# Optimization experiments

Hardware: AMD Instinct MI355X
Metric: run time of the kernel (lower is better)

## Reference

```python
import jax, jax.numpy as jnp
import numpy as np

B, N, C = 2, 2048, 1024
H = 16
D = C // H  # 64
EPS = 1e-6


def rms_norm(x, w):
    # LlamaRMSNorm: fp32 variance over last dim
    xf = x.astype(jnp.float32)
    var = jnp.mean(xf * xf, axis=-1, keepdims=True)
    xf = xf * jax.lax.rsqrt(var + EPS)
    return (w * xf).astype(x.dtype)


def setup_inputs() -> dict:
    key = jax.random.key(0)
    ks = jax.random.split(key, 4)
    x = jax.random.normal(ks[0], (B, N, C), dtype=jnp.float32)
    mask = jax.random.randint(ks[1], (B, N), 0, 2, dtype=jnp.int32)
    qkv_w = jax.random.normal(ks[2], (3 * C, C), dtype=jnp.float32) * (1.0 / np.sqrt(C))
    qkv_b = jnp.zeros((3 * C,), dtype=jnp.float32)
    proj_w = jax.random.normal(ks[3], (C, C), dtype=jnp.float32) * (1.0 / np.sqrt(C))
    proj_b = jnp.zeros((C,), dtype=jnp.float32)
    qn_w = jnp.ones((D,), dtype=jnp.float32)
    kn_w = jnp.ones((D,), dtype=jnp.float32)
    return {"x": x, "mask": mask, "qkv_w": qkv_w, "qkv_b": qkv_b,
            "proj_w": proj_w, "proj_b": proj_b, "qn_w": qn_w, "kn_w": kn_w}


def reference(x, mask, qkv_w, qkv_b, proj_w, proj_b, qn_w, kn_w):
    dtype = x.dtype
    scale = D ** -0.5
    # qkv projection -> (3, B, H, N, D)
    qkv = (x @ qkv_w.T + qkv_b).reshape(B, N, 3, H, D).transpose(2, 0, 3, 1, 4)
    q, k, v = qkv[0], qkv[1], qkv[2]
    q = rms_norm(q, qn_w)
    k = rms_norm(k, kn_w)
    q = q * scale
    # scores in fp32, key-padding mask [B,1,1,N]
    attn = jnp.einsum('bhnd,bhmd->bhnm', q, k).astype(jnp.float32)
    key_mask = (mask != 0)[:, None, None, :]
    attn = jnp.where(key_mask, attn, jnp.float32(-1e9))
    attn = jax.nn.softmax(attn, axis=-1).astype(dtype)
    out = jnp.einsum('bhnm,bhmd->bhnd', attn, v)  # (B,H,N,D)
    out = out.transpose(0, 2, 1, 3).reshape(B, N, C)
    return out @ proj_w.T + proj_b
```

## Files before the change

kernel.cpp:

```cpp
#include <hip/hip_runtime.h>
#include <hip/hip_bf16.h>
#include <stdint.h>
#include <math.h>

namespace {

constexpr int kB = 2;
constexpr int kN = 2048;
constexpr int kC = 1024;
constexpr int kH = 16;
constexpr int kD = 64;
constexpr int kTok = kB * kN;
constexpr int k3C  = 3 * kC;
constexpr size_t kPS = (size_t)kTok * k3C;
constexpr size_t kXE = (size_t)kTok * kC;
constexpr size_t kWQ = (size_t)k3C * kC;
constexpr size_t kWP = (size_t)kC * kC;

using bhalf8 = __attribute__((ext_vector_type(8))) __bf16;
using f32x4  = __attribute__((ext_vector_type(4))) float;

__device__ inline unsigned short f2bf(float f) {
  __hip_bfloat16 h = __float2bfloat16(f);
  return *reinterpret_cast<unsigned short*>(&h);
}
__device__ inline float bf2f(unsigned short u) {
  __hip_bfloat16 h;
  *reinterpret_cast<unsigned short*>(&h) = u;
  return __bfloat162float(h);
}
__device__ inline void split2(float v, unsigned short& h, unsigned short& l) {
  const unsigned short hb = f2bf(v);
  h = hb;
  l = f2bf(v - bf2f(hb));
}

#if __has_builtin(__builtin_amdgcn_exp2f)
__device__ inline float fexp2(float x) { return __builtin_amdgcn_exp2f(x); }
#else
__device__ inline float fexp2(float x) { return __expf(x * 0.6931471805599453f); }
#endif

__device__ inline void glds16(const unsigned short* g, unsigned short* l) {
  __builtin_amdgcn_global_load_lds(
      (const __attribute__((address_space(1))) void*)g,
      (__attribute__((address_space(3))) void*)l, 16, 0, 0);
}

__device__ inline void split4(const float4 v, ushort4& hh, ushort4& ll) {
  split2(v.x, hh.x, ll.x); split2(v.y, hh.y, ll.y);
  split2(v.z, hh.z, ll.z); split2(v.w, hh.w, ll.w);
}

__global__ __launch_bounds__(256)
void prep_split(const float* __restrict__ x, const float* __restrict__ wq,
                unsigned short* __restrict__ xH, unsigned short* __restrict__ xL,
                unsigned short* __restrict__ wqH, unsigned short* __restrict__ wqL)
{
  constexpr int nX = (int)(kXE / 4);
  int i = blockIdx.x * 256 + threadIdx.x;
  const float* src;
  unsigned short *H, *L;
  if (i < nX) { src = x;  H = xH;  L = xL; }
  else        { i -= nX; src = wq; H = wqH; L = wqL; }
  const float4 v = ((const float4*)src)[i];
  ushort4 hh, ll;
  split4(v, hh, ll);
  ((ushort4*)H)[i] = hh;
  ((ushort4*)L)[i] = ll;
}

__global__ __launch_bounds__(256)
void vt_and_split(const unsigned short* __restrict__ H,
                  unsigned short* __restrict__ VTH,
                  const float* __restrict__ wp,
                  unsigned short* __restrict__ wpH,
                  unsigned short* __restrict__ wpL)
{
  if (blockIdx.x < 2048) {
    const int gw   = blockIdx.x * 4 + (threadIdx.x >> 6);
    const int lane = threadIdx.x & 63;
    const int bh   = gw >> 8;
    const int oct  = gw & 255;
    const int b = bh >> 4, h = bh & 15;
    const int tok0 = oct * 8;
    union { unsigned short u[8]; uint4 v; } ph;
    #pragma unroll
    for (int e = 0; e < 8; ++e) {
      const size_t g = (size_t)(b * kN + tok0 + e) * k3C + 2 * kC + h * kD + lane;
      ph.u[e] = H[g];
    }
    *(uint4*)(&VTH[((size_t)bh * kD + lane) * kN + tok0]) = ph.v;
  } else {
    const int i = (blockIdx.x - 2048) * 256 + threadIdx.x;
    const float4 v = ((const float4*)wp)[i];
    ushort4 hh, ll;
    split4(v, hh, ll);
    ((ushort4*)wpH)[i] = hh;
    ((ushort4*)wpL)[i] = ll;
  }
}

__global__ __launch_bounds__(512)
void gemm_qkv256(const unsigned short* __restrict__ AH,
                 const unsigned short* __restrict__ AL,
                 const unsigned short* __restrict__ WH,
                 const unsigned short* __restrict__ WL,
                 const float* __restrict__ bias,
                 unsigned short* __restrict__ OutH,
                 unsigned short* __restrict__ OutL,
                 const float* __restrict__ qn,
                 const float* __restrict__ kn)
{
  constexpr int BK = 32;
  constexpr int NT = kC / BK;

  __shared__ __align__(16) unsigned short sA[2][2][256 * 32];
  __shared__ __align__(16) unsigned short sB[2][2][256 * 32];

  const int tt   = threadIdx.x;
  const int wave = tt >> 6;
  const int lane = tt & 63;
  const int quad = lane >> 4;
  const int l16  = lane & 15;
  const int bm = blockIdx.x * 256;
  const int bn = blockIdx.y * 256;
  const int wm = (wave >> 2) * 128;
  const int wn = (wave & 3) * 64;

  int srow[2], scol[2];
  #pragma unroll
  for (int r = 0; r < 2; ++r) {
    const int u = r * 512 + tt;
    srow[r] = u >> 2;
    scol[r] = ((u & 3) ^ ((srow[r] >> 1) & 3)) * 8;
  }

  auto stageU = [&](int bf, int k0, int which) {
    const unsigned short* src = (which == 0) ? AH : (which == 1) ? WH
                              : (which == 2) ? WL : AL;
    const int base = (which == 0 || which == 3) ? bm : bn;
    unsigned short* dst = (which == 0) ? &sA[bf][0][0]
                        : (which == 3) ? &sA[bf][1][0]
                        : (which == 1) ? &sB[bf][0][0] : &sB[bf][1][0];
    #pragma unroll
    for (int r = 0; r < 2; ++r)
      glds16(&src[(size_t)(base + srow[r]) * kC + k0 + scol[r]],
             &dst[(r * 512 + tt) * 8]);
  };

  auto rdA = [&](int bf, int pl, int row) -> bhalf8 {
    return *(const bhalf8*)(&sA[bf][pl][row * 32 + ((quad ^ ((row >> 1) & 3)) * 8)]);
  };
  auto rdB = [&](int bf, int pl, int row) -> bhalf8 {
    return *(const bhalf8*)(&sB[bf][pl][row * 32 + ((quad ^ ((row >> 1) & 3)) * 8)]);
  };

  f32x4 acc[8][4] = {};
  bhalf8 ah[8], bh_[4], bl_[4];

  stageU(0, 0, 0); stageU(0, 0, 1); stageU(0, 0, 2); stageU(0, 0, 3);
  asm volatile("s_waitcnt vmcnt(4)" ::: "memory");
  __builtin_amdgcn_sched_barrier(0);
  asm volatile("s_barrier" ::: "memory");

  for (int t = 0; t < NT - 1; ++t) {
    const int buf  = t & 1;
    const int nbuf = buf ^ 1;
    const int nk0  = (t + 1) * BK;

    #pragma unroll
    for (int i = 0; i < 8; ++i) ah[i]  = rdA(buf, 0, wm + i * 16 + l16);
    #pragma unroll
    for (int j = 0; j < 4; ++j) bh_[j] = rdB(buf, 0, wn + j * 16 + l16);
    stageU(nbuf, nk0, 0);
    stageU(nbuf, nk0, 1);
    asm volatile("s_waitcnt vmcnt(6)" ::: "memory");
    __builtin_amdgcn_sched_barrier(0);
    asm volatile("s_barrier" ::: "memory");
    __builtin_amdgcn_s_setprio(1);
    #pragma unroll
    for (int i = 0; i < 8; ++i)
      #pragma unroll
      for (int j = 0; j < 4; ++j)
        acc[i][j] = __builtin_amdgcn_mfma_f32_16x16x32_bf16(ah[i], bh_[j], acc[i][j], 0, 0, 0);
    __builtin_amdgcn_s_setprio(0);

    #pragma unroll
    for (int j = 0; j < 4; ++j) bl_[j] = rdB(buf, 1, wn + j * 16 + l16);
    stageU(nbuf, nk0, 2);
    asm volatile("s_waitcnt vmcnt(6)" ::: "memory");
    __builtin_amdgcn_sched_barrier(0);
    asm volatile("s_barrier" ::: "memory");
    __builtin_amdgcn_s_setprio(1);
    #pragma unroll
    for (int i = 0; i < 8; ++i)
      #pragma unroll
      for (int j = 0; j < 4; ++j)
        acc[i][j] = __builtin_amdgcn_mfma_f32_16x16x32_bf16(ah[i], bl_[j], acc[i][j], 0, 0, 0);
    __builtin_amdgcn_s_setprio(0);

    stageU(nbuf, nk0, 3);
    asm volatile("s_waitcnt vmcnt(4)" ::: "memory");
    __builtin_amdgcn_sched_barrier(0);
    asm volatile("s_barrier" ::: "memory");
    __builtin_amdgcn_s_setprio(1);
    {
      bhalf8 al0[4];
      #pragma unroll
      for (int i = 0; i < 4; ++i) al0[i] = rdA(buf, 1, wm + i * 16 + l16);
      #pragma unroll
      for (int i = 0; i < 4; ++i)
        #pragma unroll
        for (int j = 0; j < 4; ++j)
          acc[i][j] = __builtin_amdgcn_mfma_f32_16x16x32_bf16(al0[i], bh_[j], acc[i][j], 0, 0, 0);
      bhalf8 al1[4];
      #pragma unroll
      for (int i = 0; i < 4; ++i) al1[i] = rdA(buf, 1, wm + (4 + i) * 16 + l16);
      #pragma unroll
      for (int i = 0; i < 4; ++i)
        #pragma unroll
        for (int j = 0; j < 4; ++j)
          acc[4 + i][j] = __builtin_amdgcn_mfma_f32_16x16x32_bf16(al1[i], bh_[j], acc[4 + i][j], 0, 0, 0);
    }
    __builtin_amdgcn_s_setprio(0);
    asm volatile("s_barrier" ::: "memory");
  }

  {
    const int buf = (NT - 1) & 1;
    #pragma unroll
    for (int i = 0; i < 8; ++i) ah[i]  = rdA(buf, 0, wm + i * 16 + l16);
    #pragma unroll
    for (int j = 0; j < 4; ++j) bh_[j] = rdB(buf, 0, wn + j * 16 + l16);
    __builtin_amdgcn_s_setprio(1);
    #pragma unroll
    for (int i = 0; i < 8; ++i)
      #pragma unroll
      for (int j = 0; j < 4; ++j)
        acc[i][j] = __builtin_amdgcn_mfma_f32_16x16x32_bf16(ah[i], bh_[j], acc[i][j], 0, 0, 0);
    __builtin_amdgcn_s_setprio(0);

    asm volatile("s_waitcnt vmcnt(2)" ::: "memory");
    __builtin_amdgcn_sched_barrier(0);
    asm volatile("s_barrier" ::: "memory");
    #pragma unroll
    for (int j = 0; j < 4; ++j) bl_[j] = rdB(buf, 1, wn + j * 16 + l16);
    __builtin_amdgcn_s_setprio(1);
    #pragma unroll
    for (int i = 0; i < 8; ++i)
      #pragma unroll
      for (int j = 0; j < 4; ++j)
        acc[i][j] = __builtin_amdgcn_mfma_f32_16x16x32_bf16(ah[i], bl_[j], acc[i][j], 0, 0, 0);
    __builtin_amdgcn_s_setprio(0);

    asm volatile("s_waitcnt vmcnt(0)" ::: "memory");
    __builtin_amdgcn_sched_barrier(0);
    asm volatile("s_barrier" ::: "memory");
    __builtin_amdgcn_s_setprio(1);
    {
      bhalf8 al0[4];
      #pragma unroll
      for (int i = 0; i < 4; ++i) al0[i] = rdA(buf, 1, wm + i * 16 + l16);
      #pragma unroll
      for (int i = 0; i < 4; ++i)
        #pragma unroll
        for (int j = 0; j < 4; ++j)
          acc[i][j] = __builtin_amdgcn_mfma_f32_16x16x32_bf16(al0[i], bh_[j], acc[i][j], 0, 0, 0);
      bhalf8 al1[4];
      #pragma unroll
      for (int i = 0; i < 4; ++i) al1[i] = rdA(buf, 1, wm + (4 + i) * 16 + l16);
      #pragma unroll
      for (int i = 0; i < 4; ++i)
        #pragma unroll
        for (int j = 0; j < 4; ++j)
          acc[4 + i][j] = __builtin_amdgcn_mfma_f32_16x16x32_bf16(al1[i], bh_[j], acc[4 + i][j], 0, 0, 0);
    }
    __builtin_amdgcn_s_setprio(0);
  }

  const int slice = bn >> 10;
  const bool writeL = (slice == 0);
  float bv[4], wv[4];
  #pragma unroll
  for (int j = 0; j < 4; ++j) {
    bv[j] = bias[bn + wn + j * 16 + l16];
    if (slice < 2) wv[j] = (slice ? kn : qn)[j * 16 + l16];
  }

  #pragma unroll
  for (int i = 0; i < 8; ++i) {
    float val[4][4];
    #pragma unroll
    for (int j = 0; j < 4; ++j)
      #pragma unroll
      for (int r = 0; r < 4; ++r)
        val[j][r] = acc[i][j][r] + bv[j];

    if (slice < 2) {
      #pragma unroll
      for (int r = 0; r < 4; ++r) {
        float ss = val[0][r] * val[0][r];
        #pragma unroll
        for (int j = 1; j < 4; ++j) ss += val[j][r] * val[j][r];
        #pragma unroll
        for (int d = 1; d < 16; d <<= 1) ss += __shfl_xor(ss, d, 64);
        float rinv = rsqrtf(ss * (1.0f / 64.0f) + 1e-6f);
        if (slice == 0) rinv *= 0.18033688011112042f;
        #pragma unroll
        for (int j = 0; j < 4; ++j) val[j][r] = wv[j] * (val[j][r] * rinv);
      }
    }

    #pragma unroll
    for (int j = 0; j < 4; ++j) {
      const int n = bn + wn + j * 16 + l16;
      #pragma unroll
      for (int r = 0; r < 4; ++r) {
        const int m = bm + wm + i * 16 + quad * 4 + r;
        unsigned short hh, ll;
        split2(val[j][r], hh, ll);
        OutH[(size_t)m * k3C + n] = hh;
        if (writeL) OutL[(size_t)m * k3C + n] = ll;
      }
    }
  }
}

template<bool OUTF32, bool FUSE_NORM>
__global__ __launch_bounds__(256)
void gemm_planes(const unsigned short* __restrict__ AH,
                 const unsigned short* __restrict__ AL, int lda,
                 const unsigned short* __restrict__ WH,
                 const unsigned short* __restrict__ WL,
                 const float* __restrict__ bias,
                 float* __restrict__ OutF,
                 unsigned short* __restrict__ OutH,
                 unsigned short* __restrict__ OutL,
                 const float* __restrict__ qn,
                 const float* __restrict__ kn,
                 int Nn, int K)
{
  __shared__ __align__(16) unsigned short AsH[128 * 32], AsL[128 * 32];
  __shared__ __align__(16) unsigned short BsH[128 * 32], BsL[128 * 32];

  const int t    = threadIdx.x;
  const int wave = t >> 6;
  const int lane = t & 63;
  const int quad = lane >> 4;
  const int l16  = lane & 15;
  const int bm = blockIdx.x * 128;
  const int bn = blockIdx.y * 128;
  const int wm = (wave >> 1) * 64;
  const int wn = (wave & 1) * 64;

  f32x4 acc[4][4] = {};

  for (int k0 = 0; k0 < K; k0 += 32) {
    #pragma unroll
    for (int r = 0; r < 2; ++r) {
      const int c   = r * 256 + t;
      const int row = c >> 2;
      const int col = (c & 3) * 8;
      glds16(&AH[(size_t)(bm + row) * lda + k0 + col], &AsH[c * 8]);
      glds16(&AL[(size_t)(bm + row) * lda + k0 + col], &AsL[c * 8]);
      glds16(&WH[(size_t)(bn + row) * K + k0 + col], &BsH[c * 8]);
      glds16(&WL[(size_t)(bn + row) * K + k0 + col], &BsL[c * 8]);
    }
    __syncthreads();

    bhalf8 afh[4], afl[4], bgh[4], bgl[4];
    #pragma unroll
    for (int i = 0; i < 4; ++i) {
      afh[i] = *(const bhalf8*)(&AsH[(wm + i * 16 + l16) * 32 + quad * 8]);
      afl[i] = *(const bhalf8*)(&AsL[(wm + i * 16 + l16) * 32 + quad * 8]);
      bgh[i] = *(const bhalf8*)(&BsH[(wn + i * 16 + l16) * 32 + quad * 8]);
      bgl[i] = *(const bhalf8*)(&BsL[(wn + i * 16 + l16) * 32 + quad * 8]);
    }
    #pragma unroll
    for (int i = 0; i < 4; ++i)
      #pragma unroll
      for (int j = 0; j < 4; ++j) {
        f32x4 a = acc[i][j];
        a = __builtin_amdgcn_mfma_f32_16x16x32_bf16(afh[i], bgh[j], a, 0, 0, 0);
        a = __builtin_amdgcn_mfma_f32_16x16x32_bf16(afh[i], bgl[j], a, 0, 0, 0);
        a = __builtin_amdgcn_mfma_f32_16x16x32_bf16(afl[i], bgh[j], a, 0, 0, 0);
        acc[i][j] = a;
      }
    __syncthreads();
  }

  float bv[4], wv[4];
  const int slice = FUSE_NORM ? (bn >> 10) : 0;
  const bool writeL = !FUSE_NORM || slice == 0;
  #pragma unroll
  for (int j = 0; j < 4; ++j) {
    bv[j] = bias[bn + wn + j * 16 + l16];
    if (FUSE_NORM && slice < 2)
      wv[j] = (slice ? kn : qn)[j * 16 + l16];
  }

  #pragma unroll
  for (int i = 0; i < 4; ++i) {
    float val[4][4];
    #pragma unroll
    for (int j = 0; j < 4; ++j)
      #pragma unroll
      for (int r = 0; r < 4; ++r)
        val[j][r] = acc[i][j][r] + bv[j];

    if (FUSE_NORM && slice < 2) {
      #pragma unroll
      for (int r = 0; r < 4; ++r) {
        float ss = val[0][r] * val[0][r];
        #pragma unroll
        for (int j = 1; j < 4; ++j) ss += val[j][r] * val[j][r];
        #pragma unroll
        for (int d = 1; d < 16; d <<= 1) ss += __shfl_xor(ss, d, 64);
        float rinv = rsqrtf(ss * (1.0f / 64.0f) + 1e-6f);
        if (slice == 0) rinv *= 0.125f;
        #pragma unroll
        for (int j = 0; j < 4; ++j) val[j][r] = wv[j] * (val[j][r] * rinv);
      }
    }

    #pragma unroll
    for (int j = 0; j < 4; ++j) {
      const int n = bn + wn + j * 16 + l16;
      #pragma unroll
      for (int r = 0; r < 4; ++r) {
        const int m = bm + wm + i * 16 + quad * 4 + r;
        if (OUTF32) {
          OutF[(size_t)m * Nn + n] = val[j][r];
        } else {
          unsigned short hh, ll;
          split2(val[j][r], hh, ll);
          OutH[(size_t)m * Nn + n] = hh;
          if (writeL) OutL[(size_t)m * Nn + n] = ll;
        }
      }
    }
  }
}

__global__ __launch_bounds__(256)
void attn_kernel(unsigned short* __restrict__ H, unsigned short* __restrict__ L,
                 const unsigned short* __restrict__ VTH,
                 const int* __restrict__ mask)
{
  constexpr int P   = 72;
  constexpr int Ppt = 68;
  __shared__ __align__(16) unsigned short KtH[2][64 * P];
  __shared__ __align__(16) unsigned short VtH[2][64 * P];
  __shared__ __align__(16) unsigned short Pt[4][32 * Ppt];

  const int t    = threadIdx.x;
  const int wave = t >> 6;
  const int lane = t & 63;
  const int quad = lane >> 4;
  const int l16  = lane & 15;

  const int lin  = blockIdx.x;
  const int xcd  = lin & 7;
  const int slot = lin >> 3;
  const int bh   = xcd + 8 * (slot >> 4);
  const int qblk = slot & 15;
  const int b  = bh >> 4;
  const int h  = bh & 15;
  const int q0 = qblk * 128 + wave * 32;

  const int row0 = t >> 3,         col0 = (t & 7) * 8;
  const int row1 = (256 + t) >> 3, col1 = ((256 + t) & 7) * 8;

  bhalf8 qfh[2][2], qfl[2][2];
  #pragma unroll
  for (int g = 0; g < 2; ++g) {
    const size_t qrow = (size_t)(b * kN + q0 + g * 16 + l16) * k3C + h * kD;
    qfh[g][0] = *(const bhalf8*)(&H[qrow + quad * 8]);
    qfh[g][1] = *(const bhalf8*)(&H[qrow + 32 + quad * 8]);
    qfl[g][0] = *(const bhalf8*)(&L[qrow + quad * 8]);
    qfl[g][1] = *(const bhalf8*)(&L[qrow + 32 + quad * 8]);
  }

  f32x4 acc_o[2][4] = {};
  float lpart[2][4] = {};

  uint4 sk0, sk1, sv0, sv1;
  int mcur[4], mnext[4];

  auto pref = [&](int kt) {
    sk0 = *(const uint4*)(&H[(size_t)(b * kN + kt + row0) * k3C + kC + h * kD + col0]);
    sk1 = *(const uint4*)(&H[(size_t)(b * kN + kt + row1) * k3C + kC + h * kD + col1]);
    sv0 = *(const uint4*)(&VTH[((size_t)bh * kD + row0) * kN + kt + col0]);
    sv1 = *(const uint4*)(&VTH[((size_t)bh * kD + row1) * kN + kt + col1]);
  };
  auto store_tile = [&](int bf) {
    *(uint4*)(&KtH[bf][row0 * P + col0]) = sk0;
    *(uint4*)(&KtH[bf][row1 * P + col1]) = sk1;
    *(uint4*)(&VtH[bf][row0 * P + col0]) = sv0;
    *(uint4*)(&VtH[bf][row1 * P + col1]) = sv1;
  };
  auto loadM = [&](int kt, int* m) {
    #pragma unroll
    for (int nt = 0; nt < 4; ++nt) m[nt] = mask[b * kN + kt + nt * 16 + l16];
  };

  pref(0);
  loadM(0, mcur);
  #pragma unroll
  for (int nt = 0; nt < 4; ++nt) mnext[nt] = mcur[nt];
  store_tile(0);
  pref(64);
  __syncthreads();

  for (int i = 0; i < 32; ++i) {
    const int cur = i & 1;
    const int kt = i * 64;
    if (i < 31) loadM(kt + 64, mnext);

    #pragma unroll
    for (int nt = 0; nt < 4; ++nt) {
      const int kr = (nt * 16 + l16) * P + quad * 8;
      const bhalf8 kh0 = *(const bhalf8*)(&KtH[cur][kr]);
      const bhalf8 kh1 = *(const bhalf8*)(&KtH[cur][kr + 32]);
      const float flag = mcur[nt] ? 1.0f : 0.0f;
      #pragma unroll
      for (int g = 0; g < 2; ++g) {
        f32x4 s = {};
        s = __builtin_amdgcn_mfma_f32_16x16x32_bf16(qfh[g][0], kh0, s, 0, 0, 0);
        s = __builtin_amdgcn_mfma_f32_16x16x32_bf16(qfh[g][1], kh1, s, 0, 0, 0);
        s = __builtin_amdgcn_mfma_f32_16x16x32_bf16(qfl[g][0], kh0, s, 0, 0, 0);
        s = __builtin_amdgcn_mfma_f32_16x16x32_bf16(qfl[g][1], kh1, s, 0, 0, 0);
        #pragma unroll
        for (int r = 0; r < 4; ++r) {
          const float p = flag * fexp2(s[r]);
          lpart[g][r] += p;
          Pt[wave][(g * 16 + quad * 4 + r) * Ppt + nt * 16 + l16] = f2bf(p);
        }
      }
    }

    #pragma unroll
    for (int kk = 0; kk < 2; ++kk) {
      const bhalf8 pa0 = *(const bhalf8*)(&Pt[wave][l16 * Ppt + kk * 32 + quad * 8]);
      const bhalf8 pa1 = *(const bhalf8*)(&Pt[wave][(16 + l16) * Ppt + kk * 32 + quad * 8]);
      #pragma unroll
      for (int dt = 0; dt < 4; ++dt) {
        const bhalf8 vb = *(const bhalf8*)(&VtH[cur][(dt * 16 + l16) * P + kk * 32 + quad * 8]);
        acc_o[0][dt] = __builtin_amdgcn_mfma_f32_16x16x32_bf16(pa0, vb, acc_o[0][dt], 0, 0, 0);
        acc_o[1][dt] = __builtin_amdgcn_mfma_f32_16x16x32_bf16(pa1, vb, acc_o[1][dt], 0, 0, 0);
      }
    }

    if (i < 31) {
      store_tile(cur ^ 1);
      if (i < 30) pref(kt + 128);
      __syncthreads();
      #pragma unroll
      for (int nt = 0; nt < 4; ++nt) mcur[nt] = mnext[nt];
    }
  }

  #pragma unroll
  for (int g = 0; g < 2; ++g)
    #pragma unroll
    for (int r = 0; r < 4; ++r) {
      float s = lpart[g][r];
      #pragma unroll
      for (int d = 1; d < 16; d <<= 1) s += __shfl_xor(s, d, 64);
      lpart[g][r] = s;
    }
  #pragma unroll
  for (int g = 0; g < 2; ++g)
    #pragma unroll
    for (int dt = 0; dt < 4; ++dt)
      #pragma unroll
      for (int r = 0; r < 4; ++r) {
        const int qrow = q0 + g * 16 + quad * 4 + r;
        const float inv = 1.0f / fmaxf(lpart[g][r], 1.0e-30f);
        const size_t off = (size_t)(b * kN + qrow) * k3C + h * kD + dt * 16 + l16;
        unsigned short hh, ll;
        split2(acc_o[g][dt][r] * inv, hh, ll);
        H[off] = hh; L[off] = ll;
      }
}

}

extern "C" void kernel_launch(void* const* d_in, const int* in_sizes, int n_in,
                              void* d_out, int out_size, void* d_ws, size_t ws_size,
                              hipStream_t stream)
{
  const float* x      = (const float*)d_in[0];
  const int*   maskp  = (const int*)d_in[1];
  const float* qkv_w  = (const float*)d_in[2];
  const float* qkv_b  = (const float*)d_in[3];
  const float* proj_w = (const float*)d_in[4];
  const float* proj_b = (const float*)d_in[5];
  const float* qn_w   = (const float*)d_in[6];
  const float* kn_w   = (const float*)d_in[7];
  float* out = (float*)d_out;

  unsigned short* qH = (unsigned short*)d_ws;
  unsigned short* qL = qH + kPS;
  unsigned short* R1 = qL + kPS;
  unsigned short* R2 = R1 + 2 * kXE;
  unsigned short* xH = R1,  *xL = R1 + kXE;
  unsigned short* VTH = R1;
  unsigned short* wqH = R2, *wqL = R2 + kWQ;
  unsigned short* wpH = R2, *wpL = R2 + kWP;

  prep_split<<<(int)((kXE + kWQ) / 4 / 256), 256, 0, stream>>>(
      x, qkv_w, xH, xL, wqH, wqL);

  gemm_qkv256<<<dim3(kTok / 256, k3C / 256), 512, 0, stream>>>(
      xH, xL, wqH, wqL, qkv_b, qH, qL, qn_w, kn_w);

  vt_and_split<<<3072, 256, 0, stream>>>(qH, VTH, proj_w, wpH, wpL);

  attn_kernel<<<dim3(512), 256, 0, stream>>>(qH, qL, VTH, maskp);

  gemm_planes<true, false><<<dim3(kTok / 128, kC / 128), 256, 0, stream>>>(
      qH, qL, k3C, wpH, wpL, proj_b, out, nullptr, nullptr, nullptr, nullptr, kC, kC);
}
```

Measured before the change: 289.4 us.

## Double-buffer and swizzle LDS in output projection GEMM with staged plane loads

Replaces the generic templated plane GEMM used for the output projection with a specialized kernel. It double-buffers the LDS tiles and issues the next tile's four bf16 planes in stages between the three MFMA passes. Fine-grained vmcnt waits and barriers let global-to-LDS loads overlap compute. It also XOR-swizzles LDS columns to reduce bank conflicts and raises wave priority around the MFMA bursts. The cost is twice the LDS per block, which may cut occupancy, and hand-written waitcnt logic that is fragile to get right.

```diff
diff --git a/kernel.cpp b/kernel.cpp
--- a/kernel.cpp
+++ b/kernel.cpp
@@ -327,26 +327,23 @@
   }
 }
 
-template<bool OUTF32, bool FUSE_NORM>
 __global__ __launch_bounds__(256)
-void gemm_planes(const unsigned short* __restrict__ AH,
-                 const unsigned short* __restrict__ AL, int lda,
-                 const unsigned short* __restrict__ WH,
-                 const unsigned short* __restrict__ WL,
-                 const float* __restrict__ bias,
-                 float* __restrict__ OutF,
-                 unsigned short* __restrict__ OutH,
-                 unsigned short* __restrict__ OutL,
-                 const float* __restrict__ qn,
-                 const float* __restrict__ kn,
-                 int Nn, int K)
+void gemm_proj128(const unsigned short* __restrict__ AH,
+                  const unsigned short* __restrict__ AL,
+                  const unsigned short* __restrict__ WH,
+                  const unsigned short* __restrict__ WL,
+                  const float* __restrict__ bias,
+                  float* __restrict__ Out)
 {
-  __shared__ __align__(16) unsigned short AsH[128 * 32], AsL[128 * 32];
-  __shared__ __align__(16) unsigned short BsH[128 * 32], BsL[128 * 32];
-
-  const int t    = threadIdx.x;
-  const int wave = t >> 6;
-  const int lane = t & 63;
+  constexpr int BK = 32;
+  constexpr int NT = kC / BK;
+
+  __shared__ __align__(16) unsigned short sA[2][2][128 * 32];
+  __shared__ __align__(16) unsigned short sB[2][2][128 * 32];
+
+  const int tt   = threadIdx.x;
+  const int wave = tt >> 6;
+  const int lane = tt & 63;
   const int quad = lane >> 4;
   const int l16  = lane & 15;
   const int bm = blockIdx.x * 128;
@@ -354,93 +351,158 @@
   const int wm = (wave >> 1) * 64;
   const int wn = (wave & 1) * 64;
 
+  int srow[2], scol[2];
+  #pragma unroll
+  for (int r = 0; r < 2; ++r) {
+    const int c = r * 256 + tt;
+    srow[r] = c >> 2;
+    scol[r] = ((c & 3) ^ ((srow[r] >> 1) & 3)) * 8;
+  }
+
+  auto stageU = [&](int bf, int k0, int which) {
+    const unsigned short* src = (which == 0) ? AH : (which == 1) ? WH
+                              : (which == 2) ? WL : AL;
+    const bool isA = (which == 0 || which == 3);
+    const int base = isA ? bm : bn;
+    const int ld   = isA ? k3C : kC;
+    unsigned short* dst = (which == 0) ? &sA[bf][0][0]
+                        : (which == 3) ? &sA[bf][1][0]
+                        : (which == 1) ? &sB[bf][0][0] : &sB[bf][1][0];
+    #pragma unroll
+    for (int r = 0; r < 2; ++r)
+      glds16(&src[(size_t)(base + srow[r]) * ld + k0 + scol[r]],
+             &dst[(r * 256 + tt) * 8]);
+  };
+
+  auto rdA = [&](int bf, int pl, int row) -> bhalf8 {
+    return *(const bhalf8*)(&sA[bf][pl][row * 32 + ((quad ^ ((row >> 1) & 3)) * 8)]);
+  };
+  auto rdB = [&](int bf, int pl, int row) -> bhalf8 {
+    return *(const bhalf8*)(&sB[bf][pl][row * 32 + ((quad ^ ((row >> 1) & 3)) * 8)]);
+  };
+
   f32x4 acc[4][4] = {};
-
-  for (int k0 = 0; k0 < K; k0 += 32) {
-    #pragma unroll
-    for (int r = 0; r < 2; ++r) {
-      const int c   = r * 256 + t;
-      const int row = c >> 2;
-      const int col = (c & 3) * 8;
-      glds16(&AH[(size_t)(bm + row) * lda + k0 + col], &AsH[c * 8]);
-      glds16(&AL[(size_t)(bm + row) * lda + k0 + col], &AsL[c * 8]);
-      glds16(&WH[(size_t)(bn + row) * K + k0 + col], &BsH[c * 8]);
-      glds16(&WL[(size_t)(bn + row) * K + k0 + col], &BsL[c * 8]);
-    }
-    __syncthreads();
-
-    bhalf8 afh[4], afl[4], bgh[4], bgl[4];
-    #pragma unroll
-    for (int i = 0; i < 4; ++i) {
-      afh[i] = *(const bhalf8*)(&AsH[(wm + i * 16 + l16) * 32 + quad * 8]);
-      afl[i] = *(const bhalf8*)(&AsL[(wm + i * 16 + l16) * 32 + quad * 8]);
-      bgh[i] = *(const bhalf8*)(&BsH[(wn + i * 16 + l16) * 32 + quad * 8]);
-      bgl[i] = *(const bhalf8*)(&BsL[(wn + i * 16 + l16) * 32 + quad * 8]);
-    }
+  bhalf8 ah[4], bh_[4], bl_[4];
+
+  stageU(0, 0, 0); stageU(0, 0, 1); stageU(0, 0, 2); stageU(0, 0, 3);
+  asm volatile("s_waitcnt vmcnt(4)" ::: "memory");
+  __builtin_amdgcn_sched_barrier(0);
+  asm volatile("s_barrier" ::: "memory");
+
+  for (int t = 0; t < NT - 1; ++t) {
+    const int buf  = t & 1;
+    const int nbuf = buf ^ 1;
+    const int nk0  = (t + 1) * BK;
+
+    #pragma unroll
+    for (int i = 0; i < 4; ++i) ah[i]  = rdA(buf, 0, wm + i * 16 + l16);
+    #pragma unroll
+    for (int j = 0; j < 4; ++j) bh_[j] = rdB(buf, 0, wn + j * 16 + l16);
+    stageU(nbuf, nk0, 0);
+    stageU(nbuf, nk0, 1);
+    asm volatile("s_waitcnt vmcnt(6)" ::: "memory");
+    __builtin_amdgcn_sched_barrier(0);
+    asm volatile("s_barrier" ::: "memory");
+    __builtin_amdgcn_s_setprio(1);
     #pragma unroll
     for (int i = 0; i < 4; ++i)
       #pragma unroll
-      for (int j = 0; j < 4; ++j) {
-        f32x4 a = acc[i][j];
-        a = __builtin_amdgcn_mfma_f32_16x16x32_bf16(afh[i], bgh[j], a, 0, 0, 0);
-        a = __builtin_amdgcn_mfma_f32_16x16x32_bf16(afh[i], bgl[j], a, 0, 0, 0);
-        a = __builtin_amdgcn_mfma_f32_16x16x32_bf16(afl[i], bgh[j], a, 0, 0, 0);
-        acc[i][j] = a;
-      }
-    __syncthreads();
-  }
-
-  float bv[4], wv[4];
-  const int slice = FUSE_NORM ? (bn >> 10) : 0;
-  const bool writeL = !FUSE_NORM || slice == 0;
-  #pragma unroll
-  for (int j = 0; j < 4; ++j) {
-    bv[j] = bias[bn + wn + j * 16 + l16];
-    if (FUSE_NORM && slice < 2)
-      wv[j] = (slice ? kn : qn)[j * 16 + l16];
-  }
-
-  #pragma unroll
-  for (int i = 0; i < 4; ++i) {
-    float val[4][4];
-    #pragma unroll
-    for (int j = 0; j < 4; ++j)
-      #pragma unroll
-      for (int r = 0; r < 4; ++r)
-        val[j][r] = acc[i][j][r] + bv[j];
-
-    if (FUSE_NORM && slice < 2) {
-      #pragma unroll
-      for (int r = 0; r < 4; ++r) {
-        float ss = val[0][r] * val[0][r];
-        #pragma unroll
-        for (int j = 1; j < 4; ++j) ss += val[j][r] * val[j][r];
-        #pragma unroll
-        for (int d = 1; d < 16; d <<= 1) ss += __shfl_xor(ss, d, 64);
-        float rinv = rsqrtf(ss * (1.0f / 64.0f) + 1e-6f);
-        if (slice == 0) rinv *= 0.125f;
-        #pragma unroll
-        for (int j = 0; j < 4; ++j) val[j][r] = wv[j] * (val[j][r] * rinv);
-      }
-    }
-
+      for (int j = 0; j < 4; ++j)
+        acc[i][j] = __builtin_amdgcn_mfma_f32_16x16x32_bf16(ah[i], bh_[j], acc[i][j], 0, 0, 0);
+    __builtin_amdgcn_s_setprio(0);
+
+    #pragma unroll
+    for (int j = 0; j < 4; ++j) bl_[j] = rdB(buf, 1, wn + j * 16 + l16);
+    stageU(nbuf, nk0, 2);
+    asm volatile("s_waitcnt vmcnt(6)" ::: "memory");
+    __builtin_amdgcn_sched_barrier(0);
+    asm volatile("s_barrier" ::: "memory");
+    __builtin_amdgcn_s_setprio(1);
+    #pragma unroll
+    for (int i = 0; i < 4; ++i)
+      #pragma unroll
+      for (int j = 0; j < 4; ++j)
+        acc[i][j] = __builtin_amdgcn_mfma_f32_16x16x32_bf16(ah[i], bl_[j], acc[i][j], 0, 0, 0);
+    __builtin_amdgcn_s_setprio(0);
+
+    stageU(nbuf, nk0, 3);
+    asm volatile("s_waitcnt vmcnt(4)" ::: "memory");
+    __builtin_amdgcn_sched_barrier(0);
+    asm volatile("s_barrier" ::: "memory");
+    __builtin_amdgcn_s_setprio(1);
+    {
+      bhalf8 al0[4];
+      #pragma unroll
+      for (int i = 0; i < 4; ++i) al0[i] = rdA(buf, 1, wm + i * 16 + l16);
+      #pragma unroll
+      for (int i = 0; i < 4; ++i)
+        #pragma unroll
+        for (int j = 0; j < 4; ++j)
+          acc[i][j] = __builtin_amdgcn_mfma_f32_16x16x32_bf16(al0[i], bh_[j], acc[i][j], 0, 0, 0);
+    }
+    __builtin_amdgcn_s_setprio(0);
+    asm volatile("s_barrier" ::: "memory");
+  }
+
+  {
+    const int buf = (NT - 1) & 1;
+    #pragma unroll
+    for (int i = 0; i < 4; ++i) ah[i]  = rdA(buf, 0, wm + i * 16 + l16);
+    #pragma unroll
+    for (int j = 0; j < 4; ++j) bh_[j] = rdB(buf, 0, wn + j * 16 + l16);
+    __builtin_amdgcn_s_setprio(1);
+    #pragma unroll
+    for (int i = 0; i < 4; ++i)
+      #pragma unroll
+      for (int j = 0; j < 4; ++j)
+        acc[i][j] = __builtin_amdgcn_mfma_f32_16x16x32_bf16(ah[i], bh_[j], acc[i][j], 0, 0, 0);
+    __builtin_amdgcn_s_setprio(0);
+
+    asm volatile("s_waitcnt vmcnt(2)" ::: "memory");
+    __builtin_amdgcn_sched_barrier(0);
+    asm volatile("s_barrier" ::: "memory");
+    #pragma unroll
+    for (int j = 0; j < 4; ++j) bl_[j] = rdB(buf, 1, wn + j * 16 + l16);
+    __builtin_amdgcn_s_setprio(1);
+    #pragma unroll
+    for (int i = 0; i < 4; ++i)
+      #pragma unroll
+      for (int j = 0; j < 4; ++j)
+        acc[i][j] = __builtin_amdgcn_mfma_f32_16x16x32_bf16(ah[i], bl_[j], acc[i][j], 0, 0, 0);
+    __builtin_amdgcn_s_setprio(0);
+
+    asm volatile("s_waitcnt vmcnt(0)" ::: "memory");
+    __builtin_amdgcn_sched_barrier(0);
+    asm volatile("s_barrier" ::: "memory");
+    __builtin_amdgcn_s_setprio(1);
+    {
+      bhalf8 al0[4];
+      #pragma unroll
+      for (int i = 0; i < 4; ++i) al0[i] = rdA(buf, 1, wm + i * 16 + l16);
+      #pragma unroll
+      for (int i = 0; i < 4; ++i)
+        #pragma unroll
+        for (int j = 0; j < 4; ++j)
+          acc[i][j] = __builtin_amdgcn_mfma_f32_16x16x32_bf16(al0[i], bh_[j], acc[i][j], 0, 0, 0);
+    }
+    __builtin_amdgcn_s_setprio(0);
+  }
+
+  float bv[4];
+  #pragma unroll
+  for (int j = 0; j < 4; ++j) bv[j] = bias[bn + wn + j * 16 + l16];
+
+  #pragma unroll
+  for (int i = 0; i < 4; ++i)
     #pragma unroll
     for (int j = 0; j < 4; ++j) {
       const int n = bn + wn + j * 16 + l16;
       #pragma unroll
       for (int r = 0; r < 4; ++r) {
         const int m = bm + wm + i * 16 + quad * 4 + r;
-        if (OUTF32) {
-          OutF[(size_t)m * Nn + n] = val[j][r];
-        } else {
-          unsigned short hh, ll;
-          split2(val[j][r], hh, ll);
-          OutH[(size_t)m * Nn + n] = hh;
-          if (writeL) OutL[(size_t)m * Nn + n] = ll;
-        }
+        Out[(size_t)m * kC + n] = acc[i][j][r] + bv[j];
       }
     }
-  }
 }
 
 __global__ __launch_bounds__(256)
@@ -620,6 +682,6 @@
 
   attn_kernel<<<dim3(512), 256, 0, stream>>>(qH, qL, VTH, maskp);
 
-  gemm_planes<true, false><<<dim3(kTok / 128, kC / 128), 256, 0, stream>>>(
-      qH, qL, k3C, wpH, wpL, proj_b, out, nullptr, nullptr, nullptr, nullptr, kC, kC);
-}
+  gemm_proj128<<<dim3(kTok / 128, kC / 128), 256, 0, stream>>>(
+      qH, qL, wpH, wpL, proj_b, out);
+}
```

After: 282.1 us. 2.5% less time.
